# Kernel tuning notes

Measured on AMD Instinct MI355X. Metric: run time of the kernel, lower is better.

Reference implementation:

```python
import jax, jax.numpy as jnp
import numpy as np
from functools import partial

DIM = 1024
LIGHT_HID = 512   # dim * 0.5
HEAVY_HID = 4096  # dim * 4
NUM_HEAVY = 1024
N_ITERS = 50
K_ROUTE = 8.0
EPS = 0.1


def rms_norm(x, gamma):
    # F.normalize(x, dim=-1) * sqrt(dim) * gamma
    norm = jnp.linalg.norm(x, axis=-1, keepdims=True)
    normed = x / jnp.maximum(norm, 1e-12)
    return normed * (x.shape[-1] ** 0.5) * gamma


def ffn(x, gamma, w1, b1, w2, b2):
    h = rms_norm(x, gamma)
    h = jax.nn.gelu(h @ w1 + b1, approximate=False)
    return h @ w2 + b2


def coor_descent_route(x, routing_token, num_tokens):
    # s: [b, n]
    s = jnp.einsum('bnd,d->bn', x, routing_token)
    constant = EPS * jnp.log(jnp.asarray(K_ROUTE, dtype=s.dtype))
    b0 = -jax.nn.relu(s)
    a0 = jnp.zeros((s.shape[0], 1), dtype=s.dtype)

    def step(carry, _):
        a_prev, b = carry
        a = constant - EPS * jax.nn.logsumexp((s + b) / EPS, axis=-1, keepdims=True)
        b = -jax.nn.relu(s + a)
        return (a, b), None

    (a, b), _ = jax.lax.scan(step, (a0, b0), None, length=N_ITERS)
    scores = jnp.exp((s + a + b) / EPS)
    sel_scores, sel_idx = jax.lax.top_k(scores, num_tokens)
    # straight-through: value -> 1.0, gradient -> d(sel_scores)
    sel_scores = sel_scores + jax.lax.stop_gradient(1.0 - sel_scores)
    return sel_scores, sel_idx


def setup_inputs() -> dict:
    key = jax.random.key(0)
    ks = jax.random.split(key, 12)
    def lin(k, fan_in, fan_out):
        lim = 1.0 / np.sqrt(fan_in)
        kw, kb = jax.random.split(k)
        w = jax.random.uniform(kw, (fan_in, fan_out), jnp.float32, -lim, lim)
        b = jax.random.uniform(kb, (fan_out,), jnp.float32, -lim, lim)
        return w, b
    x = jax.random.normal(ks[0], (4, 8192, DIM), jnp.float32)
    routing_token = jax.random.normal(ks[1], (DIM,), jnp.float32)
    gamma_light = jnp.ones((DIM,), jnp.float32)
    w1_l, b1_l = lin(ks[2], DIM, LIGHT_HID)
    w2_l, b2_l = lin(ks[3], LIGHT_HID, DIM)
    gamma_heavy = jnp.ones((DIM,), jnp.float32)
    w1_h, b1_h = lin(ks[4], DIM, HEAVY_HID)
    w2_h, b2_h = lin(ks[5], HEAVY_HID, DIM)
    return dict(x=x, routing_token=routing_token,
                gamma_light=gamma_light, w1_light=w1_l, b1_light=b1_l,
                w2_light=w2_l, b2_light=b2_l,
                gamma_heavy=gamma_heavy, w1_heavy=w1_h, b1_heavy=b1_h,
                w2_heavy=w2_h, b2_heavy=b2_h)


def reference(x, routing_token, gamma_light, w1_light, b1_light, w2_light, b2_light,
              gamma_heavy, w1_heavy, b1_heavy, w2_heavy, b2_heavy):
    bsz = x.shape[0]
    light_out = ffn(x, gamma_light, w1_light, b1_light, w2_light, b2_light)
    sel_scores, sel_idx = coor_descent_route(x, routing_token, NUM_HEAVY)
    batch_range = jnp.arange(bsz)[:, None]           # [b, 1]
    routed = x[batch_range, sel_idx]                 # [b, k, d]
    routed_out = ffn(routed, gamma_heavy, w1_heavy, b1_heavy, w2_heavy, b2_heavy)
    routed_out = routed_out * sel_scores[..., None]
    heavy_out = jnp.zeros_like(x).at[batch_range, sel_idx].set(routed_out)
    return light_out + heavy_out
```

## Files before the change

### kernel.cpp

```cpp
#include <hip/hip_runtime.h>
#include <math.h>

#define TOKS   32768
#define NSEQ   8192
#define BATCH  4
#define DIMD   1024
#define LHID   512
#define HHID   4096
#define NHEAVY 1024

typedef __attribute__((ext_vector_type(8))) short bf16x8;
typedef __attribute__((ext_vector_type(4))) float f32x4;
typedef __attribute__((ext_vector_type(8))) unsigned short u16x8;
typedef __attribute__((ext_vector_type(4))) unsigned short u16x4;

__device__ __forceinline__ unsigned short bf16rne(float f) {
    unsigned u = __float_as_uint(f);
    return (unsigned short)((u + 0x7FFFu + ((u >> 16) & 1u)) >> 16);
}
__device__ __forceinline__ float gelu_f(float v) {
    return 0.5f * v * (1.0f + erff(v * 0.7071067811865476f));
}
__device__ __forceinline__ void gload_lds16(const unsigned short* g, unsigned short* l) {
#if defined(__HIP_DEVICE_COMPILE__)
    __builtin_amdgcn_global_load_lds((const __attribute__((address_space(1))) void*)g,
                                     (__attribute__((address_space(3))) void*)l,
                                     16, 0, 0);
#endif
}

__global__ __launch_bounds__(256) void k_rowscale(const float* __restrict__ x,
                                                  const float* __restrict__ rt,
                                                  const float* __restrict__ gamma,
                                                  float* __restrict__ s,
                                                  float* __restrict__ invr,
                                                  unsigned short* __restrict__ xl) {
    int wid = threadIdx.x >> 6, lane = threadIdx.x & 63;
    int row = blockIdx.x * 4 + wid;
    const float4* xr  = (const float4*)(x + (size_t)row * DIMD);
    const float4* rt4 = (const float4*)rt;
    const float4* g4  = (const float4*)gamma;
    float4 v[4];
    float dot = 0.f, ss = 0.f;
#pragma unroll
    for (int i = 0; i < 4; i++) {
        v[i] = xr[lane + 64 * i];
        float4 r = rt4[lane + 64 * i];
        dot += v[i].x * r.x + v[i].y * r.y + v[i].z * r.z + v[i].w * r.w;
        ss  += v[i].x * v[i].x + v[i].y * v[i].y + v[i].z * v[i].z + v[i].w * v[i].w;
    }
#pragma unroll
    for (int o = 32; o > 0; o >>= 1) {
        dot += __shfl_xor(dot, o);
        ss  += __shfl_xor(ss, o);
    }
    float iv = 32.0f / fmaxf(sqrtf(ss), 1e-12f);
    if (lane == 0) { s[row] = dot; invr[row] = iv; }
#pragma unroll
    for (int i = 0; i < 4; i++) {
        float4 g = g4[lane + 64 * i];
        u16x4 o;
        o[0] = bf16rne(v[i].x * iv * g.x);
        o[1] = bf16rne(v[i].y * iv * g.y);
        o[2] = bf16rne(v[i].z * iv * g.z);
        o[3] = bf16rne(v[i].w * iv * g.w);
        *(u16x4*)(xl + (size_t)row * DIMD + (lane + 64 * i) * 4) = o;
    }
}

__global__ __launch_bounds__(256) void k_rowstats(const float* __restrict__ x,
                                                  const float* __restrict__ rt,
                                                  float* __restrict__ s,
                                                  float* __restrict__ invr) {
    int wid = threadIdx.x >> 6, lane = threadIdx.x & 63;
    int row = blockIdx.x * 4 + wid;
    const float4* xr  = (const float4*)(x + (size_t)row * DIMD);
    const float4* rt4 = (const float4*)rt;
    float dot = 0.f, ss = 0.f;
#pragma unroll
    for (int i = 0; i < 4; i++) {
        float4 v = xr[lane + 64 * i];
        float4 r = rt4[lane + 64 * i];
        dot += v.x * r.x + v.y * r.y + v.z * r.z + v.w * r.w;
        ss  += v.x * v.x + v.y * v.y + v.z * v.z + v.w * v.w;
    }
#pragma unroll
    for (int o = 32; o > 0; o >>= 1) {
        dot += __shfl_down(dot, o);
        ss  += __shfl_down(ss, o);
    }
    if (lane == 0) {
        s[row] = dot;
        invr[row] = 32.0f / fmaxf(sqrtf(ss), 1e-12f);
    }
}

__global__ __launch_bounds__(1024) void k_route(const float* __restrict__ s_g,
                                                unsigned long long* __restrict__ keys,
                                                int* __restrict__ pcount,
                                                int* __restrict__ c1cnt) {
    int b = blockIdx.x, tid = threadIdx.x;
    int lane = tid & 63, wid = tid >> 6;
    const float* sb = s_g + b * NSEQ;
    float sv[8];
    float smax = -3.4e38f;
#pragma unroll
    for (int i = 0; i < 8; i++) { sv[i] = sb[tid + 1024 * i]; smax = fmaxf(smax, sv[i]); }
    __shared__ float red[2][16];
#pragma unroll
    for (int o = 32; o > 0; o >>= 1) smax = fmaxf(smax, __shfl_xor(smax, o));
    if (lane == 0) red[0][wid] = smax;
    __syncthreads();
    float smaxAll = -3.4e38f;
    for (int w = 0; w < 16; w++) smaxAll = fmaxf(smaxAll, red[0][w]);
    __syncthreads();

    const float cst = 0.1f * logf(8.0f);
    float a = 0.0f;
    for (int it = 0; it < 50; it++) {
        float tau = -a;
        float M = fminf(smaxAll, tau);
        float p = 0.0f;
#pragma unroll
        for (int i = 0; i < 8; i++) p += expf((fminf(sv[i], tau) - M) * 10.0f);
#pragma unroll
        for (int o = 32; o > 0; o >>= 1) p += __shfl_xor(p, o);
        if (lane == 0) red[it & 1][wid] = p;
        __syncthreads();
        float S = 0.0f;
        for (int w = 0; w < 16; w++) S += red[it & 1][w];
        a = cst - M - 0.1f * logf(S);
    }
    int p = 0, c1 = 0;
#pragma unroll
    for (int i = 0; i < 8; i++) {
        float sc = expf(fminf(sv[i] + a, 0.0f) * 10.0f);
        int n = tid + 1024 * i;
        keys[b * NSEQ + n] = ((unsigned long long)__float_as_uint(sc) << 32)
                           | (unsigned long long)(0xFFFFFFFFu - (unsigned)n);
        p  += (sc > 0.0f) ? 1 : 0;
        c1 += (sc == 1.0f) ? 1 : 0;
    }
#pragma unroll
    for (int o = 32; o > 0; o >>= 1) {
        p  += __shfl_xor(p, o);
        c1 += __shfl_xor(c1, o);
    }
    if (lane == 0) { atomicAdd(&pcount[b], p); atomicAdd(&c1cnt[b], c1); }
}

__global__ __launch_bounds__(1024) void k_select(const unsigned long long* __restrict__ keys,
                                                 const int* __restrict__ pcount,
                                                 const int* __restrict__ c1cnt,
                                                 int* __restrict__ rowmap) {
    int b = blockIdx.x, tid = threadIdx.x;
    int lane = tid & 63, wid = tid >> 6;
    __shared__ int wsum[16];
    __shared__ int slot;
    __shared__ unsigned long long kk_[NSEQ];
    int P = pcount[b], C1 = c1cnt[b];
    if (C1 >= NHEAVY) {
        bool f[8]; int zc = 0;
#pragma unroll
        for (int j = 0; j < 8; j++) {
            unsigned hi = (unsigned)(keys[b * NSEQ + tid * 8 + j] >> 32);
            f[j] = (hi == 0x3F800000u);
            zc += f[j] ? 1 : 0;
        }
        int inc = zc;
        for (int o = 1; o < 64; o <<= 1) {
            int t = __shfl_up(inc, o);
            if (lane >= o) inc += t;
        }
        if (lane == 63) wsum[wid] = inc;
        __syncthreads();
        if (tid == 0) {
            int acc = 0;
            for (int w = 0; w < 16; w++) { int t = wsum[w]; wsum[w] = acc; acc += t; }
        }
        __syncthreads();
        int rank = wsum[wid] + (inc - zc);
#pragma unroll
        for (int j = 0; j < 8; j++) {
            if (f[j]) {
                if (rank < NHEAVY) rowmap[b * NHEAVY + rank] = b * NSEQ + tid * 8 + j;
                rank++;
            }
        }
    } else if (P <= NHEAVY) {
        bool pos[8]; int zc = 0;
#pragma unroll
        for (int j = 0; j < 8; j++) {
            unsigned sbits = (unsigned)(keys[b * NSEQ + tid * 8 + j] >> 32);
            pos[j] = (sbits != 0u);
            zc += pos[j] ? 0 : 1;
        }
        int inc = zc;
        for (int o = 1; o < 64; o <<= 1) {
            int t = __shfl_up(inc, o);
            if (lane >= o) inc += t;
        }
        if (lane == 63) wsum[wid] = inc;
        if (tid == 0) slot = 0;
        __syncthreads();
        if (tid == 0) {
            int acc = 0;
            for (int w = 0; w < 16; w++) { int t = wsum[w]; wsum[w] = acc; acc += t; }
        }
        __syncthreads();
        int zr = wsum[wid] + (inc - zc);
        int Z = NHEAVY - P;
#pragma unroll
        for (int j = 0; j < 8; j++) {
            int n = tid * 8 + j;
            bool sel;
            if (pos[j]) sel = true;
            else { sel = (zr < Z); zr += 1; }
            if (sel) {
                int sl = atomicAdd(&slot, 1);
                rowmap[b * NHEAVY + sl] = b * NSEQ + n;
            }
        }
    } else {
        for (int i = tid; i < NSEQ; i += 1024) kk_[i] = keys[b * NSEQ + i];
        __syncthreads();
        for (int k = 2; k <= NSEQ; k <<= 1) {
            for (int j = k >> 1; j > 0; j >>= 1) {
                for (int i = tid; i < NSEQ; i += 1024) {
                    int ixj = i ^ j;
                    if (ixj > i) {
                        unsigned long long u = kk_[i], v = kk_[ixj];
                        bool dirDesc = ((i & k) == 0);
                        if (dirDesc ? (u < v) : (u > v)) { kk_[i] = v; kk_[ixj] = u; }
                    }
                }
                __syncthreads();
            }
        }
        unsigned idx = 0xFFFFFFFFu - (unsigned)(kk_[tid] & 0xFFFFFFFFull);
        rowmap[b * NHEAVY + tid] = b * NSEQ + (int)idx;
    }
}

__global__ __launch_bounds__(256) void k_transpose(const float* __restrict__ W,
                                                   unsigned short* __restrict__ WT,
                                                   int K, int N) {
    __shared__ float ts[64][65];
    int t = threadIdx.x;
    int n0 = blockIdx.x * 64, k0 = blockIdx.y * 64;
    int kk = t >> 2, nc = (t & 3) * 16;
    const float4* src = (const float4*)(W + (size_t)(k0 + kk) * N + n0 + nc);
#pragma unroll
    for (int j = 0; j < 4; j++) {
        float4 v = src[j];
        ts[kk][nc + 4 * j + 0] = v.x;
        ts[kk][nc + 4 * j + 1] = v.y;
        ts[kk][nc + 4 * j + 2] = v.z;
        ts[kk][nc + 4 * j + 3] = v.w;
    }
    __syncthreads();
    int nn = t >> 2, kc = (t & 3) * 16;
    unsigned short o[16];
#pragma unroll
    for (int j = 0; j < 16; j++) o[j] = bf16rne(ts[kc + j][nn]);
    unsigned short* dst = WT + (size_t)(n0 + nn) * K + k0 + kc;
    *(u16x8*)(dst)     = *(u16x8*)(o);
    *(u16x8*)(dst + 8) = *(u16x8*)(o + 8);
}

__global__ __launch_bounds__(256) void k_prescale(const float* __restrict__ x,
                                                  const float* __restrict__ invr,
                                                  const float* __restrict__ gamma,
                                                  const int* __restrict__ rowmap,
                                                  unsigned short* __restrict__ xo,
                                                  int row_ofs) {
    int t = threadIdx.x;
    int i = blockIdx.x * 2 + (t >> 7);
    int c = (t & 127) * 8;
    int src = rowmap ? rowmap[i] : (row_ofs + i);
    float iv = invr[src];
    const float4* px = (const float4*)(x + (size_t)src * DIMD + c);
    const float4* pg = (const float4*)(gamma + c);
    float4 v0 = px[0], v1 = px[1];
    float4 g0 = pg[0], g1 = pg[1];
    unsigned short o[8];
    o[0] = bf16rne(v0.x * iv * g0.x); o[1] = bf16rne(v0.y * iv * g0.y);
    o[2] = bf16rne(v0.z * iv * g0.z); o[3] = bf16rne(v0.w * iv * g0.w);
    o[4] = bf16rne(v1.x * iv * g1.x); o[5] = bf16rne(v1.y * iv * g1.y);
    o[6] = bf16rne(v1.z * iv * g1.z); o[7] = bf16rne(v1.w * iv * g1.w);
    *(u16x8*)(xo + (size_t)i * DIMD + c) = *(u16x8*)o;
}

template<int EPI>
__global__ __launch_bounds__(256, 2) void k_mfma(
        const unsigned short* __restrict__ A, const unsigned short* __restrict__ BT,
        const float* __restrict__ bias, void* __restrict__ Cv,
        const int* __restrict__ rowmap,
        int K, int kslice, int m_ofs, int ldc, int nx, int ny) {
    __shared__ unsigned short As[2][128 * 64];
    __shared__ unsigned short Bs[2][128 * 64];
    int tid = threadIdx.x;

    int nwg = gridDim.x, w = blockIdx.x;
    int q = nwg >> 3, r = nwg & 7;
    int xcd = w & 7, sub = w >> 3;
    int id = (xcd < r ? xcd * (q + 1) : r * (q + 1) + (xcd - r) * q) + sub;
    int bx = id % nx;
    int t2 = id / nx;
    int by = t2 % ny;
    int bz = t2 / ny;

    int m0 = by * 128, n0 = bx * 128;
    int kbeg = bz * kslice, kend = kbeg + kslice;
    int lane = tid & 63, wid = tid >> 6;
    int wm = wid >> 1, wn = wid & 1;
    int lc = lane & 15, lr = lane >> 4;

    int srow = lane >> 3;
    int sslot = (lane & 7) ^ srow;
    const unsigned short* paA = A  + (size_t)(m0 + srow) * K + sslot * 8;
    const unsigned short* paB = BT + (size_t)(n0 + srow) * K + sslot * 8;

    auto stage = [&](int buf, int kk) {
#pragma unroll
        for (int qq = 0; qq < 4; qq++) {
            int rb = (wid * 4 + qq) * 8;
            gload_lds16(paA + (size_t)rb * K + kk, &As[buf][rb * 64]);
            gload_lds16(paB + (size_t)rb * K + kk, &Bs[buf][rb * 64]);
        }
    };

    f32x4 acc[4][4];
#pragma unroll
    for (int i = 0; i < 4; i++)
#pragma unroll
        for (int j = 0; j < 4; j++) acc[i][j] = (f32x4){0.f, 0.f, 0.f, 0.f};

    stage(0, kbeg);
    for (int k0 = kbeg; k0 < kend; k0 += 64) {
        int cur = ((k0 - kbeg) >> 6) & 1;
        __syncthreads();
        if (k0 + 64 < kend) stage(cur ^ 1, k0 + 64);
        const char* baseA = (const char*)As[cur];
        const char* baseB = (const char*)Bs[cur];
#pragma unroll
        for (int ks = 0; ks < 2; ks++) {
            bf16x8 af[4], bfr[4];
#pragma unroll
            for (int f = 0; f < 4; f++) {
                int rowA = wm * 64 + f * 16 + lc;
                int rowB = wn * 64 + f * 16 + lc;
                int sw = ((ks * 4 + lr) ^ (lc & 7)) << 4;
                af[f]  = *(const bf16x8*)(baseA + rowA * 128 + sw);
                bfr[f] = *(const bf16x8*)(baseB + rowB * 128 + sw);
            }
#pragma unroll
            for (int fm = 0; fm < 4; fm++)
#pragma unroll
                for (int fn = 0; fn < 4; fn++)
                    acc[fm][fn] = __builtin_amdgcn_mfma_f32_16x16x32_bf16(
                        af[fm], bfr[fn], acc[fm][fn], 0, 0, 0);
        }
    }

    float bcol[4];
#pragma unroll
    for (int fn = 0; fn < 4; fn++) {
        float bb = bias[n0 + wn * 64 + fn * 16 + lc];
        if constexpr (EPI == 3) { if (bz != 0) bb = 0.0f; }
        bcol[fn] = bb;
    }
#pragma unroll
    for (int fm = 0; fm < 4; fm++) {
        int rowb = m0 + wm * 64 + fm * 16 + lr * 4;
#pragma unroll
        for (int fn = 0; fn < 4; fn++) {
            int col = n0 + wn * 64 + fn * 16 + lc;
            f32x4 v = acc[fm][fn];
#pragma unroll
            for (int rr = 0; rr < 4; rr++) {
                float val = v[rr] + bcol[fn];
                if constexpr (EPI == 0) {
                    ((unsigned short*)Cv)[(size_t)(rowb + rr) * ldc + col] = bf16rne(gelu_f(val));
                } else if constexpr (EPI == 1) {
                    ((float*)Cv)[(size_t)(m_ofs + rowb + rr) * ldc + col] = val;
                } else if constexpr (EPI == 2) {
                    int g = rowmap[m_ofs + rowb + rr];
                    float* p = (float*)Cv + (size_t)g * ldc + col;
                    *p = *p + val;
                } else {
                    int g = rowmap[m_ofs + rowb + rr];
                    atomicAdd((float*)Cv + (size_t)g * ldc + col, val);
                }
            }
        }
    }
}

extern "C" void kernel_launch(void* const* d_in, const int* in_sizes, int n_in,
                              void* d_out, int out_size, void* d_ws, size_t ws_size,
                              hipStream_t stream) {
    const float* x   = (const float*)d_in[0];
    const float* rt  = (const float*)d_in[1];
    const float* gl  = (const float*)d_in[2];
    const float* w1l = (const float*)d_in[3];
    const float* b1l = (const float*)d_in[4];
    const float* w2l = (const float*)d_in[5];
    const float* b2l = (const float*)d_in[6];
    const float* gh  = (const float*)d_in[7];
    const float* w1h = (const float*)d_in[8];
    const float* b1h = (const float*)d_in[9];
    const float* w2h = (const float*)d_in[10];
    const float* b2h = (const float*)d_in[11];
    float* out = (float*)d_out;

    char* ws = (char*)d_ws;
    float* s    = (float*)(ws);
    float* invr = (float*)(ws + 131072);
    unsigned long long* keys = (unsigned long long*)(ws + 262144);
    int* rowmap = (int*)(ws + 524288);
    int* pcount = (int*)(ws + 540672);
    int* c1cnt  = pcount + 4;
    size_t off = 1u << 20;
    unsigned short* w1lT = (unsigned short*)(ws + off); off += (size_t)LHID * DIMD * 2;
    unsigned short* w2lT = (unsigned short*)(ws + off); off += (size_t)DIMD * LHID * 2;
    unsigned short* w1hT = (unsigned short*)(ws + off); off += (size_t)HHID * DIMD * 2;
    unsigned short* w2hT = (unsigned short*)(ws + off); off += (size_t)DIMD * HHID * 2;
    unsigned short* xhg  = (unsigned short*)(ws + off); off += (size_t)BATCH * NHEAVY * DIMD * 2;
    char* un = ws + off;
    size_t U = ws_size > off ? ws_size - off : 0;

    const size_t XL_B = (size_t)TOKS * DIMD * 2;
    const size_t HL_B = (size_t)TOKS * LHID * 2;
    const size_t HH_B = (size_t)BATCH * NHEAVY * HHID * 2;
    bool big = (U >= XL_B + HL_B) && (U >= HH_B);

    hipMemsetAsync(pcount, 0, 32, stream);

    const long MH = (long)BATCH * NHEAVY;

    if (big) {
        unsigned short* xl = (unsigned short*)un;
        unsigned short* hl = (unsigned short*)(un + XL_B);
        unsigned short* hh = (unsigned short*)un;

        k_rowscale<<<TOKS / 4, 256, 0, stream>>>(x, rt, gl, s, invr, xl);
        k_route<<<BATCH, 1024, 0, stream>>>(s, keys, pcount, c1cnt);
        k_select<<<BATCH, 1024, 0, stream>>>(keys, pcount, c1cnt, rowmap);

        k_transpose<<<dim3(LHID / 64, DIMD / 64), 256, 0, stream>>>(w1l, w1lT, DIMD, LHID);
        k_transpose<<<dim3(DIMD / 64, LHID / 64), 256, 0, stream>>>(w2l, w2lT, LHID, DIMD);
        k_transpose<<<dim3(HHID / 64, DIMD / 64), 256, 0, stream>>>(w1h, w1hT, DIMD, HHID);
        k_transpose<<<dim3(DIMD / 64, HHID / 64), 256, 0, stream>>>(w2h, w2hT, HHID, DIMD);

        k_mfma<0><<<(LHID / 128) * (TOKS / 128), 256, 0, stream>>>(
            xl, w1lT, b1l, hl, nullptr, DIMD, DIMD, 0, LHID, LHID / 128, TOKS / 128);
        k_mfma<1><<<(DIMD / 128) * (TOKS / 128), 256, 0, stream>>>(
            hl, w2lT, b2l, out, nullptr, LHID, LHID, 0, DIMD, DIMD / 128, TOKS / 128);

        k_prescale<<<(unsigned)(MH / 2), 256, 0, stream>>>(x, invr, gh, rowmap, xhg, 0);
        k_mfma<0><<<(HHID / 128) * ((int)MH / 128), 256, 0, stream>>>(
            xhg, w1hT, b1h, hh, nullptr, DIMD, DIMD, 0, HHID, HHID / 128, (int)MH / 128);
        k_mfma<3><<<(DIMD / 128) * ((int)MH / 128) * 4, 256, 0, stream>>>(
            hh, w2hT, b2h, out, rowmap, HHID, HHID / 4, 0, DIMD, DIMD / 128, (int)MH / 128);
    } else {
        k_rowstats<<<TOKS / 4, 256, 0, stream>>>(x, rt, s, invr);
        k_route<<<BATCH, 1024, 0, stream>>>(s, keys, pcount, c1cnt);
        k_select<<<BATCH, 1024, 0, stream>>>(keys, pcount, c1cnt, rowmap);

        k_transpose<<<dim3(LHID / 64, DIMD / 64), 256, 0, stream>>>(w1l, w1lT, DIMD, LHID);
        k_transpose<<<dim3(DIMD / 64, LHID / 64), 256, 0, stream>>>(w2l, w2lT, LHID, DIMD);
        k_transpose<<<dim3(HHID / 64, DIMD / 64), 256, 0, stream>>>(w1h, w1hT, DIMD, HHID);
        k_transpose<<<dim3(DIMD / 64, HHID / 64), 256, 0, stream>>>(w2h, w2hT, HHID, DIMD);

        long Rl = (long)(U / 3072);
        Rl -= Rl % 128; if (Rl < 128) Rl = 128; if (Rl > TOKS) Rl = TOKS;
        unsigned short* xl = (unsigned short*)un;
        unsigned short* hl = (unsigned short*)(un + (size_t)Rl * DIMD * 2);
        for (long mo = 0; mo < TOKS; mo += Rl) {
            long R = TOKS - mo < Rl ? TOKS - mo : Rl;
            k_prescale<<<(unsigned)(R / 2), 256, 0, stream>>>(x, invr, gl, nullptr, xl, (int)mo);
            k_mfma<0><<<(LHID / 128) * (unsigned)(R / 128), 256, 0, stream>>>(
                xl, w1lT, b1l, hl, nullptr, DIMD, DIMD, 0, LHID, LHID / 128, (int)(R / 128));
            k_mfma<1><<<(DIMD / 128) * (unsigned)(R / 128), 256, 0, stream>>>(
                hl, w2lT, b2l, out, nullptr, LHID, LHID, (int)mo, DIMD, DIMD / 128, (int)(R / 128));
        }

        k_prescale<<<(unsigned)(MH / 2), 256, 0, stream>>>(x, invr, gh, rowmap, xhg, 0);
        long Rh = (long)(U / ((size_t)HHID * 2));
        Rh -= Rh % 128; if (Rh < 128) Rh = 128; if (Rh > MH) Rh = MH;
        unsigned short* hh = (unsigned short*)un;
        for (long mo = 0; mo < MH; mo += Rh) {
            long R = MH - mo < Rh ? MH - mo : Rh;
            k_mfma<0><<<(HHID / 128) * (unsigned)(R / 128), 256, 0, stream>>>(
                xhg + (size_t)mo * DIMD, w1hT, b1h, hh, nullptr, DIMD, DIMD, 0, HHID,
                HHID / 128, (int)(R / 128));
            k_mfma<2><<<(DIMD / 128) * (unsigned)(R / 128), 256, 0, stream>>>(
                hh, w2hT, b2h, out, rowmap, HHID, HHID, (int)mo, DIMD,
                DIMD / 128, (int)(R / 128));
        }
    }
}
```

Measured before the change: 386.1 us.

## Co-launch light and heavy GEMMs in merged grids, single-buffer LDS, scatter via buffer

The light and heavy FFN GEMMs are now merged into two combined launches: one grid runs both first-layer GEMMs, and another runs both second-layer GEMMs. The aim is to remove the tail and launch gaps between four separate kernels. The LDS staging goes from double-buffered to single-buffered with an extra barrier, which halves shared memory so four blocks fit per CU, at the cost of no load/compute overlap inside a block. Heavy-FFN split-K partial sums now go by atomics into a zeroed scratch buffer, and a separate scatter kernel then adds them into the output. This adds a memset, another kernel, and a larger workspace requirement for the fast path.

```diff
diff --git a/kernel.cpp b/kernel.cpp
--- a/kernel.cpp
+++ b/kernel.cpp
@@ -291,58 +291,64 @@
     *(u16x8*)(xo + (size_t)i * DIMD + c) = *(u16x8*)o;
 }
 
+__global__ __launch_bounds__(256) void k_scatter(const float* __restrict__ rb,
+                                                 const int* __restrict__ rowmap,
+                                                 float* __restrict__ out) {
+    int i = blockIdx.x;
+    int c = threadIdx.x * 4;
+    int g = rowmap[i];
+    float4 v = *(const float4*)(rb + (size_t)i * DIMD + c);
+    float* p = out + (size_t)g * DIMD + c;
+    float4 o = *(const float4*)p;
+    o.x += v.x; o.y += v.y; o.z += v.z; o.w += v.w;
+    *(float4*)p = o;
+}
+
+struct GArg {
+    const unsigned short* A; const unsigned short* BT; const float* bias;
+    void* C; const int* rowmap;
+    int K, kslice, m_ofs, ldc, nx, ny;
+};
+
 template<int EPI>
-__global__ __launch_bounds__(256, 2) void k_mfma(
-        const unsigned short* __restrict__ A, const unsigned short* __restrict__ BT,
-        const float* __restrict__ bias, void* __restrict__ Cv,
-        const int* __restrict__ rowmap,
-        int K, int kslice, int m_ofs, int ldc, int nx, int ny) {
-    __shared__ unsigned short As[2][128 * 64];
-    __shared__ unsigned short Bs[2][128 * 64];
+__device__ __forceinline__ void gemm_body(const GArg ga, int w, int nwg,
+                                          unsigned short* As, unsigned short* Bs) {
     int tid = threadIdx.x;
-
-    int nwg = gridDim.x, w = blockIdx.x;
     int q = nwg >> 3, r = nwg & 7;
     int xcd = w & 7, sub = w >> 3;
     int id = (xcd < r ? xcd * (q + 1) : r * (q + 1) + (xcd - r) * q) + sub;
-    int bx = id % nx;
-    int t2 = id / nx;
-    int by = t2 % ny;
-    int bz = t2 / ny;
+    int bx = id % ga.nx;
+    int t2 = id / ga.nx;
+    int by = t2 % ga.ny;
+    int bz = t2 / ga.ny;
 
     int m0 = by * 128, n0 = bx * 128;
-    int kbeg = bz * kslice, kend = kbeg + kslice;
+    int kbeg = bz * ga.kslice, kend = kbeg + ga.kslice;
+    int K = ga.K;
     int lane = tid & 63, wid = tid >> 6;
     int wm = wid >> 1, wn = wid & 1;
     int lc = lane & 15, lr = lane >> 4;
 
     int srow = lane >> 3;
     int sslot = (lane & 7) ^ srow;
-    const unsigned short* paA = A  + (size_t)(m0 + srow) * K + sslot * 8;
-    const unsigned short* paB = BT + (size_t)(n0 + srow) * K + sslot * 8;
-
-    auto stage = [&](int buf, int kk) {
+    const unsigned short* paA = ga.A  + (size_t)(m0 + srow) * K + sslot * 8;
+    const unsigned short* paB = ga.BT + (size_t)(n0 + srow) * K + sslot * 8;
+
+    f32x4 acc[4][4];
+#pragma unroll
+    for (int i = 0; i < 4; i++)
+#pragma unroll
+        for (int j = 0; j < 4; j++) acc[i][j] = (f32x4){0.f, 0.f, 0.f, 0.f};
+
+    for (int k0 = kbeg; k0 < kend; k0 += 64) {
+        if (k0 != kbeg) __syncthreads();
 #pragma unroll
         for (int qq = 0; qq < 4; qq++) {
-            int rb = (wid * 4 + qq) * 8;
-            gload_lds16(paA + (size_t)rb * K + kk, &As[buf][rb * 64]);
-            gload_lds16(paB + (size_t)rb * K + kk, &Bs[buf][rb * 64]);
-        }
-    };
-
-    f32x4 acc[4][4];
-#pragma unroll
-    for (int i = 0; i < 4; i++)
-#pragma unroll
-        for (int j = 0; j < 4; j++) acc[i][j] = (f32x4){0.f, 0.f, 0.f, 0.f};
-
-    stage(0, kbeg);
-    for (int k0 = kbeg; k0 < kend; k0 += 64) {
-        int cur = ((k0 - kbeg) >> 6) & 1;
-        __syncthreads();
-        if (k0 + 64 < kend) stage(cur ^ 1, k0 + 64);
-        const char* baseA = (const char*)As[cur];
-        const char* baseB = (const char*)Bs[cur];
+            int rb_ = (wid * 4 + qq) * 8;
+            gload_lds16(paA + (size_t)rb_ * K + k0, &As[rb_ * 64]);
+            gload_lds16(paB + (size_t)rb_ * K + k0, &Bs[rb_ * 64]);
+        }
+        __syncthreads();
 #pragma unroll
         for (int ks = 0; ks < 2; ks++) {
             bf16x8 af[4], bfr[4];
@@ -351,8 +357,8 @@
                 int rowA = wm * 64 + f * 16 + lc;
                 int rowB = wn * 64 + f * 16 + lc;
                 int sw = ((ks * 4 + lr) ^ (lc & 7)) << 4;
-                af[f]  = *(const bf16x8*)(baseA + rowA * 128 + sw);
-                bfr[f] = *(const bf16x8*)(baseB + rowB * 128 + sw);
+                af[f]  = *(const bf16x8*)((const char*)As + rowA * 128 + sw);
+                bfr[f] = *(const bf16x8*)((const char*)Bs + rowB * 128 + sw);
             }
 #pragma unroll
             for (int fm = 0; fm < 4; fm++)
@@ -366,7 +372,7 @@
     float bcol[4];
 #pragma unroll
     for (int fn = 0; fn < 4; fn++) {
-        float bb = bias[n0 + wn * 64 + fn * 16 + lc];
+        float bb = ga.bias[n0 + wn * 64 + fn * 16 + lc];
         if constexpr (EPI == 3) { if (bz != 0) bb = 0.0f; }
         bcol[fn] = bb;
     }
@@ -381,20 +387,35 @@
             for (int rr = 0; rr < 4; rr++) {
                 float val = v[rr] + bcol[fn];
                 if constexpr (EPI == 0) {
-                    ((unsigned short*)Cv)[(size_t)(rowb + rr) * ldc + col] = bf16rne(gelu_f(val));
+                    ((unsigned short*)ga.C)[(size_t)(rowb + rr) * ga.ldc + col] =
+                        bf16rne(gelu_f(val));
                 } else if constexpr (EPI == 1) {
-                    ((float*)Cv)[(size_t)(m_ofs + rowb + rr) * ldc + col] = val;
+                    ((float*)ga.C)[(size_t)(ga.m_ofs + rowb + rr) * ga.ldc + col] = val;
                 } else if constexpr (EPI == 2) {
-                    int g = rowmap[m_ofs + rowb + rr];
-                    float* p = (float*)Cv + (size_t)g * ldc + col;
+                    int g = ga.rowmap[ga.m_ofs + rowb + rr];
+                    float* p = (float*)ga.C + (size_t)g * ga.ldc + col;
                     *p = *p + val;
                 } else {
-                    int g = rowmap[m_ofs + rowb + rr];
-                    atomicAdd((float*)Cv + (size_t)g * ldc + col, val);
+                    int g = ga.rowmap ? ga.rowmap[rowb + rr] : (rowb + rr);
+                    atomicAdd((float*)ga.C + (size_t)g * ga.ldc + col, val);
                 }
             }
         }
     }
+}
+
+template<int EPI>
+__global__ __launch_bounds__(256, 4) void k_mfma(GArg ga) {
+    __shared__ unsigned short sm[2][128 * 64];
+    gemm_body<EPI>(ga, (int)blockIdx.x, (int)gridDim.x, sm[0], sm[1]);
+}
+
+template<int EA, int EB>
+__global__ __launch_bounds__(256, 4) void k_mfma2(GArg a, GArg b, int nwgA) {
+    __shared__ unsigned short sm[2][128 * 64];
+    int w = (int)blockIdx.x;
+    if (w < nwgA) gemm_body<EA>(a, w, nwgA, sm[0], sm[1]);
+    else          gemm_body<EB>(b, w - nwgA, (int)gridDim.x - nwgA, sm[0], sm[1]);
 }
 
 extern "C" void kernel_launch(void* const* d_in, const int* in_sizes, int n_in,
@@ -433,7 +454,7 @@
     const size_t XL_B = (size_t)TOKS * DIMD * 2;
     const size_t HL_B = (size_t)TOKS * LHID * 2;
     const size_t HH_B = (size_t)BATCH * NHEAVY * HHID * 2;
-    bool big = (U >= XL_B + HL_B) && (U >= HH_B);
+    bool big = (U >= XL_B + HL_B + HH_B);
 
     hipMemsetAsync(pcount, 0, 32, stream);
 
@@ -442,7 +463,8 @@
     if (big) {
         unsigned short* xl = (unsigned short*)un;
         unsigned short* hl = (unsigned short*)(un + XL_B);
-        unsigned short* hh = (unsigned short*)un;
+        unsigned short* hh = (unsigned short*)(un + XL_B + HL_B);
+        float* rb = (float*)un;
 
         k_rowscale<<<TOKS / 4, 256, 0, stream>>>(x, rt, gl, s, invr, xl);
         k_route<<<BATCH, 1024, 0, stream>>>(s, keys, pcount, c1cnt);
@@ -452,17 +474,18 @@
         k_transpose<<<dim3(DIMD / 64, LHID / 64), 256, 0, stream>>>(w2l, w2lT, LHID, DIMD);
         k_transpose<<<dim3(HHID / 64, DIMD / 64), 256, 0, stream>>>(w1h, w1hT, DIMD, HHID);
         k_transpose<<<dim3(DIMD / 64, HHID / 64), 256, 0, stream>>>(w2h, w2hT, HHID, DIMD);
-
-        k_mfma<0><<<(LHID / 128) * (TOKS / 128), 256, 0, stream>>>(
-            xl, w1lT, b1l, hl, nullptr, DIMD, DIMD, 0, LHID, LHID / 128, TOKS / 128);
-        k_mfma<1><<<(DIMD / 128) * (TOKS / 128), 256, 0, stream>>>(
-            hl, w2lT, b2l, out, nullptr, LHID, LHID, 0, DIMD, DIMD / 128, TOKS / 128);
-
         k_prescale<<<(unsigned)(MH / 2), 256, 0, stream>>>(x, invr, gh, rowmap, xhg, 0);
-        k_mfma<0><<<(HHID / 128) * ((int)MH / 128), 256, 0, stream>>>(
-            xhg, w1hT, b1h, hh, nullptr, DIMD, DIMD, 0, HHID, HHID / 128, (int)MH / 128);
-        k_mfma<3><<<(DIMD / 128) * ((int)MH / 128) * 4, 256, 0, stream>>>(
-            hh, w2hT, b2h, out, rowmap, HHID, HHID / 4, 0, DIMD, DIMD / 128, (int)MH / 128);
+
+        GArg lg1{xl,  w1lT, b1l, hl, nullptr, DIMD, DIMD, 0, LHID, LHID / 128, TOKS / 128};
+        GArg hg1{xhg, w1hT, b1h, hh, nullptr, DIMD, DIMD, 0, HHID, HHID / 128, (int)MH / 128};
+        k_mfma2<0, 0><<<2048, 256, 0, stream>>>(lg1, hg1, 1024);
+
+        hipMemsetAsync(rb, 0, (size_t)MH * DIMD * 4, stream);
+        GArg lg2{hl, w2lT, b2l, out, nullptr, LHID, LHID, 0, DIMD, DIMD / 128, TOKS / 128};
+        GArg hg2{hh, w2hT, b2h, rb, nullptr, HHID, HHID / 4, 0, DIMD, DIMD / 128, (int)MH / 128};
+        k_mfma2<1, 3><<<3072, 256, 0, stream>>>(lg2, hg2, 2048);
+
+        k_scatter<<<(unsigned)MH, 256, 0, stream>>>(rb, rowmap, out);
     } else {
         k_rowstats<<<TOKS / 4, 256, 0, stream>>>(x, rt, s, invr);
         k_route<<<BATCH, 1024, 0, stream>>>(s, keys, pcount, c1cnt);
@@ -480,10 +503,10 @@
         for (long mo = 0; mo < TOKS; mo += Rl) {
             long R = TOKS - mo < Rl ? TOKS - mo : Rl;
             k_prescale<<<(unsigned)(R / 2), 256, 0, stream>>>(x, invr, gl, nullptr, xl, (int)mo);
-            k_mfma<0><<<(LHID / 128) * (unsigned)(R / 128), 256, 0, stream>>>(
-                xl, w1lT, b1l, hl, nullptr, DIMD, DIMD, 0, LHID, LHID / 128, (int)(R / 128));
-            k_mfma<1><<<(DIMD / 128) * (unsigned)(R / 128), 256, 0, stream>>>(
-                hl, w2lT, b2l, out, nullptr, LHID, LHID, (int)mo, DIMD, DIMD / 128, (int)(R / 128));
+            GArg a1{xl, w1lT, b1l, hl, nullptr, DIMD, DIMD, 0, LHID, LHID / 128, (int)(R / 128)};
+            k_mfma<0><<<(LHID / 128) * (unsigned)(R / 128), 256, 0, stream>>>(a1);
+            GArg a2{hl, w2lT, b2l, out, nullptr, LHID, LHID, (int)mo, DIMD, DIMD / 128, (int)(R / 128)};
+            k_mfma<1><<<(DIMD / 128) * (unsigned)(R / 128), 256, 0, stream>>>(a2);
         }
 
         k_prescale<<<(unsigned)(MH / 2), 256, 0, stream>>>(x, invr, gh, rowmap, xhg, 0);
@@ -492,12 +515,12 @@
         unsigned short* hh = (unsigned short*)un;
         for (long mo = 0; mo < MH; mo += Rh) {
             long R = MH - mo < Rh ? MH - mo : Rh;
-            k_mfma<0><<<(HHID / 128) * (unsigned)(R / 128), 256, 0, stream>>>(
-                xhg + (size_t)mo * DIMD, w1hT, b1h, hh, nullptr, DIMD, DIMD, 0, HHID,
-                HHID / 128, (int)(R / 128));
-            k_mfma<2><<<(DIMD / 128) * (unsigned)(R / 128), 256, 0, stream>>>(
-                hh, w2hT, b2h, out, rowmap, HHID, HHID, (int)mo, DIMD,
-                DIMD / 128, (int)(R / 128));
-        }
-    }
-}
+            GArg b1{xhg + (size_t)mo * DIMD, w1hT, b1h, hh, nullptr, DIMD, DIMD, 0, HHID,
+                    HHID / 128, (int)(R / 128)};
+            k_mfma<0><<<(HHID / 128) * (unsigned)(R / 128), 256, 0, stream>>>(b1);
+            GArg b2{hh, w2hT, b2h, out, rowmap, HHID, HHID, (int)mo, DIMD,
+                    DIMD / 128, (int)(R / 128)};
+            k_mfma<2><<<(DIMD / 128) * (unsigned)(R / 128), 256, 0, stream>>>(b2);
+        }
+    }
+}
```

Measured after the change: 392.8 us. About the same (+1.7%).
